# Kernel optimization log

Measured on AMD Instinct MI355X. Metric: run time of the kernel, lower is better.

Reference implementation:

```python
import jax, jax.numpy as jnp
import numpy as np

B, SQ, SKV = 4, 4096, 1024
QDIM, CDIM = 1024, 768
HEADS, DHEAD = 16, 64
INNER = HEADS * DHEAD


def setup_inputs() -> dict:
    key = jax.random.key(0)
    ks = jax.random.split(key, 7)
    s = 0.02
    return {
        "x": jax.random.normal(ks[0], (B, SQ, QDIM), dtype=jnp.float32),
        "context": jax.random.normal(ks[1], (B, SKV, CDIM), dtype=jnp.float32),
        "Wq": jax.random.normal(ks[2], (QDIM, INNER), dtype=jnp.float32) * s,
        "Wk": jax.random.normal(ks[3], (CDIM, INNER), dtype=jnp.float32) * s,
        "Wv": jax.random.normal(ks[4], (CDIM, INNER), dtype=jnp.float32) * s,
        "Wo": jax.random.normal(ks[5], (INNER, QDIM), dtype=jnp.float32) * s,
        "bo": jnp.zeros((QDIM,), dtype=jnp.float32),
    }


def reference(x, context, Wq, Wk, Wv, Wo, bo):
    # QKV projections (no bias, matching bias=False Linear layers)
    q = x @ Wq          # [B, SQ, INNER]
    k = context @ Wk    # [B, SKV, INNER]
    v = context @ Wv    # [B, SKV, INNER]

    # split heads: b s (h d) -> b h s d
    def split_heads(t, s):
        return t.reshape(B, s, HEADS, DHEAD).transpose(0, 2, 1, 3)

    qh = split_heads(q, SQ)
    kh = split_heads(k, SKV)
    vh = split_heads(v, SKV)

    scale = DHEAD ** -0.5  # attention_basic default scale
    sim = jnp.einsum('bhqd,bhkd->bhqk', qh, kh) * scale  # [B,H,SQ,SKV]
    attn = jax.nn.softmax(sim, axis=-1)
    out = jnp.einsum('bhqk,bhkd->bhqd', attn, vh)        # [B,H,SQ,DHEAD]
    out = out.transpose(0, 2, 1, 3).reshape(B, SQ, INNER)

    # output projection (Linear with bias); dropout p=0 -> identity
    return out @ Wo + bo
```

## Files before the change

### kernel.cpp

```cpp
#include <hip/hip_runtime.h>


typedef unsigned short u16;
typedef unsigned int u32;
typedef __bf16 bf16x8 __attribute__((ext_vector_type(8)));
typedef float float4v __attribute__((ext_vector_type(4)));
typedef _Float16 half4 __attribute__((ext_vector_type(4)));
typedef _Float16 half2v __attribute__((ext_vector_type(2)));
typedef __attribute__((address_space(1))) void as1_void;
typedef __attribute__((address_space(3))) void as3_void;

__device__ __forceinline__ u16 f2bf(float f) {
  unsigned u = __float_as_uint(f);
  u += 0x7FFF + ((u >> 16) & 1);
  return (u16)(u >> 16);
}

__device__ __forceinline__ void async16(const u16* g, u16* l) {
  __builtin_amdgcn_global_load_lds((as1_void*)(void*)g, (as3_void*)l, 16, 0, 0);
}

#define WAITCNT_VM8 0xF78
#define WAITCNT_VM4 0xF74
#define WAITCNT_VM0 0xF70

__global__ void cvt_kernel(const float* __restrict__ x, u16* __restrict__ xbf,
                           const float* __restrict__ ctx, u16* __restrict__ ctxbf) {
  int i = blockIdx.x * 256 + threadIdx.x;
  const float* in; u16* out; int j;
  if (i < 4194304) { in = x; out = xbf; j = i; }
  else if (i < 4980736) { in = ctx; out = ctxbf; j = i - 4194304; }
  else return;
  float4 v = ((const float4*)in)[j];
  ushort4 o;
  o.x = f2bf(v.x); o.y = f2bf(v.y); o.z = f2bf(v.z); o.w = f2bf(v.w);
  ((ushort4*)out)[j] = o;
}

__global__ void twt_kernel(const float* __restrict__ Wq, const float* __restrict__ Wk,
                           const float* __restrict__ Wv, const float* __restrict__ Wo,
                           u16* __restrict__ WqT, u16* __restrict__ WkT,
                           u16* __restrict__ WvT, u16* __restrict__ WoT) {
  __shared__ u16 t[32][33];
  int z = blockIdx.z;
  const float* W = z == 0 ? Wq : z == 1 ? Wk : z == 2 ? Wv : Wo;
  u16* Wt = z == 0 ? WqT : z == 1 ? WkT : z == 2 ? WvT : WoT;
  int Kd = (z == 1 || z == 2) ? 768 : 1024;
  int k0 = blockIdx.y * 32;
  if (k0 >= Kd) return;
  int tx = threadIdx.x, ty = threadIdx.y;
  int n0 = blockIdx.x * 32;
#pragma unroll
  for (int i = 0; i < 4; i++)
    t[ty + i * 8][tx] = f2bf(W[(size_t)(k0 + ty + i * 8) * 1024 + n0 + tx]);
  __syncthreads();
#pragma unroll
  for (int i = 0; i < 4; i++)
    Wt[(size_t)(n0 + ty + i * 8) * Kd + k0 + tx] = t[tx][ty + i * 8];
}


__device__ __forceinline__ void ld_a4(const u16* Lp, int rbase, int quad,
                                      int l15, bf16x8 a[4][2]) {
  int lb = l15 & 7;
  const char* base = (const char*)Lp;
#pragma unroll
  for (int mi = 0; mi < 4; mi++)
#pragma unroll
    for (int ks = 0; ks < 2; ks++)
      a[mi][ks] = *(const bf16x8*)(base + (rbase + mi * 16 + l15) * 128 +
                                   (((ks * 4 + quad) ^ lb) << 4));
}

__device__ __forceinline__ void ld_b2(const u16* Lp, int rbase, int quad,
                                      int l15, bf16x8 b[2][2]) {
  int lb = l15 & 7;
  const char* base = (const char*)Lp;
#pragma unroll
  for (int ni = 0; ni < 2; ni++)
#pragma unroll
    for (int ks = 0; ks < 2; ks++)
      b[ni][ks] = *(const bf16x8*)(base + (rbase + ni * 16 + l15) * 128 +
                                   (((ks * 4 + quad) ^ lb) << 4));
}

__device__ __forceinline__ void mm16(bf16x8 a[4][2], bf16x8 b[2][2],
                                     float4v acc[8][4], int mh, int nh) {
  __builtin_amdgcn_s_setprio(1);
#pragma unroll
  for (int mi = 0; mi < 4; mi++)
#pragma unroll
    for (int ni = 0; ni < 2; ni++)
#pragma unroll
      for (int ks = 0; ks < 2; ks++)
        acc[mh * 4 + mi][nh * 2 + ni] = __builtin_amdgcn_mfma_f32_16x16x32_bf16(
            a[mi][ks], b[ni][ks], acc[mh * 4 + mi][nh * 2 + ni], 0, 0, 0);
  __builtin_amdgcn_s_setprio(0);
}

__device__ __forceinline__ void gemm256_core(const u16* __restrict__ A,
                                             const u16* __restrict__ Bt, int K,
                                             int m0, int n0, float4v acc[8][4]) {
  __shared__ __align__(16) u16 L[2][2][256][64];
  int tid = threadIdx.x;
  int w = tid >> 6, lane = tid & 63;
  int l15 = lane & 15, quad = lane >> 4;
  int wm = (w >> 2) * 128, wn = (w & 3) * 64;

  int lr = lane >> 3, sl = lane & 7;
  const u16* pA = A + (size_t)(m0 + (w << 5) + lr) * K + ((sl ^ lr) << 3);
  const u16* pB = Bt + (size_t)(n0 + (w << 5) + lr) * K + ((sl ^ lr) << 3);
  size_t r8 = (size_t)K << 3;
  int dofs = (w << 11) + lane * 8;

#define STG_A(buf, t)                                                          \
  do {                                                                         \
    const u16* s = pA + (size_t)(t) * 64;                                      \
    u16* d = &L[buf][0][0][0] + dofs;                                          \
    async16(s, d);                                                             \
    async16(s + r8, d + 512);                                                  \
    async16(s + 2 * r8, d + 1024);                                             \
    async16(s + 3 * r8, d + 1536);                                             \
  } while (0)
#define STG_B(buf, t)                                                          \
  do {                                                                         \
    const u16* s = pB + (size_t)(t) * 64;                                      \
    u16* d = &L[buf][1][0][0] + dofs;                                          \
    async16(s, d);                                                             \
    async16(s + r8, d + 512);                                                  \
    async16(s + 2 * r8, d + 1024);                                             \
    async16(s + 3 * r8, d + 1536);                                             \
  } while (0)

  STG_A(0, 0); STG_B(0, 0);
  STG_A(1, 1); STG_B(1, 1);
  __builtin_amdgcn_s_waitcnt(WAITCNT_VM8);
  __builtin_amdgcn_s_barrier();

  bf16x8 a[4][2], b0[2][2], b1[2][2];
  int I = K >> 7;
  for (int i = 0; i < I; ++i) {
    int st = (i + 1 < I);
    ld_a4(&L[0][0][0][0], wm, quad, l15, a);
    ld_b2(&L[0][1][0][0], wn, quad, l15, b0);
    if (i > 0) STG_B(1, 2 * i + 1);
    __builtin_amdgcn_s_barrier();
    mm16(a, b0, acc, 0, 0);
    __builtin_amdgcn_s_barrier();
    ld_b2(&L[0][1][0][0], wn + 32, quad, l15, b1);
    __builtin_amdgcn_s_barrier();
    mm16(a, b1, acc, 0, 1);
    __builtin_amdgcn_s_barrier();
    ld_a4(&L[0][0][0][0], wm + 64, quad, l15, a);
    __builtin_amdgcn_s_barrier();
    mm16(a, b1, acc, 1, 1);
    __builtin_amdgcn_s_barrier();
    if (st) STG_A(0, 2 * i + 2);
    __builtin_amdgcn_s_barrier();
    mm16(a, b0, acc, 1, 0);
    if (st) __builtin_amdgcn_s_waitcnt(WAITCNT_VM4);
    else    __builtin_amdgcn_s_waitcnt(WAITCNT_VM0);
    __builtin_amdgcn_s_barrier();
    ld_a4(&L[1][0][0][0], wm, quad, l15, a);
    ld_b2(&L[1][1][0][0], wn, quad, l15, b0);
    if (st) STG_B(0, 2 * i + 2);
    __builtin_amdgcn_s_barrier();
    mm16(a, b0, acc, 0, 0);
    __builtin_amdgcn_s_barrier();
    ld_b2(&L[1][1][0][0], wn + 32, quad, l15, b1);
    __builtin_amdgcn_s_barrier();
    mm16(a, b1, acc, 0, 1);
    __builtin_amdgcn_s_barrier();
    ld_a4(&L[1][0][0][0], wm + 64, quad, l15, a);
    __builtin_amdgcn_s_barrier();
    mm16(a, b1, acc, 1, 1);
    __builtin_amdgcn_s_barrier();
    if (st) STG_A(1, 2 * i + 3);
    __builtin_amdgcn_s_barrier();
    mm16(a, b0, acc, 1, 0);
    if (st) __builtin_amdgcn_s_waitcnt(WAITCNT_VM4);
    __builtin_amdgcn_s_barrier();
  }
#undef STG_A
#undef STG_B
}

__global__ __launch_bounds__(512, 2) void qkv_gemm8(
    const u16* __restrict__ xbf, const u16* __restrict__ ctxbf,
    const u16* __restrict__ WqT, const u16* __restrict__ WkT, const u16* __restrict__ WvT,
    u16* __restrict__ Qb, u16* __restrict__ Kbuf, u16* __restrict__ Vtb, float qscale) {
  int bx0 = blockIdx.x;
  int bx = (bx0 & 7) * 48 + (bx0 >> 3);
  const u16* A; const u16* Bt; u16* C; int K, mode, m0, n0; float scale;
  if (bx < 256)      { int t = bx;       A = xbf;   Bt = WqT; C = Qb;   K = 1024; mode = 0; scale = qscale; m0 = (t >> 2) * 256; n0 = (t & 3) * 256; }
  else if (bx < 320) { int t = bx - 256; A = ctxbf; Bt = WkT; C = Kbuf; K = 768;  mode = 0; scale = 1.0f;   m0 = (t >> 2) * 256; n0 = (t & 3) * 256; }
  else               { int t = bx - 320; A = ctxbf; Bt = WvT; C = Vtb;  K = 768;  mode = 2; scale = 1.0f;   m0 = (t >> 2) * 256; n0 = (t & 3) * 256; }

  float4v acc[8][4] = {};
  gemm256_core(A, Bt, K, m0, n0, acc);

  int tid = threadIdx.x;
  int w = tid >> 6, lane = tid & 63;
  int l15 = lane & 15, quad = lane >> 4;
  int wm = (w >> 2) * 128, wn = (w & 3) * 64;

  if (mode == 0) {
#pragma unroll
    for (int mi = 0; mi < 8; mi++) {
      int rowb = m0 + wm + mi * 16 + quad * 4;
#pragma unroll
      for (int ni = 0; ni < 4; ni++) {
        int col = n0 + wn + ni * 16 + l15;
#pragma unroll
        for (int r = 0; r < 4; r++)
          C[(size_t)(rowb + r) * 1024 + col] = f2bf(acc[mi][ni][r] * scale);
      }
    }
  } else {
#pragma unroll
    for (int mi = 0; mi < 8; mi++) {
      int rowb = m0 + wm + mi * 16 + quad * 4;
#pragma unroll
      for (int ni = 0; ni < 4; ni++) {
        int col = n0 + wn + ni * 16 + l15;
        int hh = col >> 6, dd = col & 63;
#pragma unroll
        for (int r = 0; r < 4; r++) {
          int rr = rowb + r;
          int b = rr >> 10, skv = rr & 1023;
          _Float16 hv = (_Float16)acc[mi][ni][r];
          C[((((size_t)b * 16 + hh) * 64 + dd) << 10) + skv] = __builtin_bit_cast(u16, hv);
        }
      }
    }
  }
}

__global__ __launch_bounds__(512, 2) void gemm_bt8(
    const u16* __restrict__ A, const u16* __restrict__ Bt,
    float* __restrict__ C, const float* __restrict__ bias) {
  int bx0 = blockIdx.x;
  int bx = (bx0 & 7) * 32 + (bx0 >> 3);
  int m0 = (bx >> 2) * 256, n0 = (bx & 3) * 256;

  float4v acc[8][4] = {};
  gemm256_core(A, Bt, 1024, m0, n0, acc);

  int tid = threadIdx.x;
  int w = tid >> 6, lane = tid & 63;
  int l15 = lane & 15, quad = lane >> 4;
  int wm = (w >> 2) * 128, wn = (w & 3) * 64;

#pragma unroll
  for (int mi = 0; mi < 8; mi++) {
    int rowb = m0 + wm + mi * 16 + quad * 4;
#pragma unroll
    for (int ni = 0; ni < 4; ni++) {
      int col = n0 + wn + ni * 16 + l15;
      float bv = bias[col];
#pragma unroll
      for (int r = 0; r < 4; r++)
        C[(size_t)(rowb + r) * 1024 + col] = acc[mi][ni][r] + bv;
    }
  }
}

__global__ __launch_bounds__(512, 4) void attn_kernel(
    const u16* __restrict__ Q, const u16* __restrict__ Kb,
    const u16* __restrict__ Vt, u16* __restrict__ Oout) {
  __shared__ __align__(16) u16 lK[2][8192];
  __shared__ __align__(16) u16 lV[2][8192];
  int tid = threadIdx.x, w = tid >> 6, lane = tid & 63;
  int l15 = lane & 15, quad = lane >> 4;
  int bh = blockIdx.y, b = bh >> 4, h = bh & 15;
  int q0 = blockIdx.x * 256 + w * 32;

  const u16* Qbase = Q + ((size_t)(b * 4096 + q0)) * 1024 + h * 64;
  const u16* Kbase = Kb + ((size_t)b << 20) + h * 64;
  const u16* Vbase = Vt + ((size_t)bh << 16);

  bf16x8 qf[2][2];
#pragma unroll
  for (int qt = 0; qt < 2; qt++)
#pragma unroll
    for (int c = 0; c < 2; c++)
      qf[qt][c] = *(const bf16x8*)(Qbase + (size_t)(qt * 16 + l15) * 1024 + c * 32 + quad * 8);

  int kr0 = tid >> 3, kx0 = ((tid & 7) ^ (kr0 & 7)) * 8;
  const u16* ks0 = Kbase + (size_t)kr0 * 1024 + kx0;
  const u16* ks1 = ks0 + (size_t)64 * 1024;
  int vd0 = tid >> 4, vc0 = ((tid & 15) ^ (vd0 & 15)) * 8;
  const u16* vs0 = Vbase + (size_t)vd0 * 1024 + vc0;
  const u16* vs1 = vs0 + (size_t)32 * 1024;
  int kdo0 = w * 512, kdo1 = 4096 + w * 512;

  async16(ks0, &lK[0][kdo0]); async16(ks1, &lK[0][kdo1]);
  async16(vs0, &lV[0][kdo0]); async16(vs1, &lV[0][kdo1]);
  ks0 += 131072; ks1 += 131072;
  vs0 += 128; vs1 += 128;

  float4v o[2][4] = {};
  float4v osum[2] = {};
  const half4 ones = {(_Float16)1.0f, (_Float16)1.0f, (_Float16)1.0f, (_Float16)1.0f};

  int lb = l15 & 7;
  int xk0 = ((0 + quad) ^ lb) * 16 + l15 * 128;
  int xk1 = ((4 + quad) ^ lb) * 16 + l15 * 128;
  int qh = quad >> 1, qo = (quad & 1) * 8;
  int vrow = l15 * 256 + qo;

  for (int it = 0; it < 8; ++it) {
    const char* bK = (const char*)lK + (it & 1) * 16384;
    const char* bV = (const char*)lV + (it & 1) * 16384;
    __syncthreads();
    if (it < 7) {
      int nb = (it + 1) & 1;
      async16(ks0, &lK[nb][kdo0]); async16(ks1, &lK[nb][kdo1]);
      async16(vs0, &lV[nb][kdo0]); async16(vs1, &lV[nb][kdo1]);
      ks0 += 131072; ks1 += 131072;
      vs0 += 128; vs1 += 128;
    }
#pragma unroll
    for (int ss = 0; ss < 8; ss++) {
      int sub = (ss + w) & 7;
      int sb = sub * 2048;
      float4v sv[2] = {{0.f, 0.f, 0.f, 0.f}, {0.f, 0.f, 0.f, 0.f}};
      __builtin_amdgcn_s_setprio(1);
#pragma unroll
      for (int c = 0; c < 2; c++) {
        bf16x8 kf = *(const bf16x8*)(bK + sb + (c ? xk1 : xk0));
#pragma unroll
        for (int qt = 0; qt < 2; qt++)
          sv[qt] = __builtin_amdgcn_mfma_f32_16x16x32_bf16(kf, qf[qt][c], sv[qt], 0, 0, 0);
      }
      __builtin_amdgcn_s_setprio(0);
      half4 pf[2];
#pragma unroll
      for (int qt = 0; qt < 2; qt++) {
        float e0 = exp2f(sv[qt][0]), e1 = exp2f(sv[qt][1]);
        float e2 = exp2f(sv[qt][2]), e3 = exp2f(sv[qt][3]);
        half2v p01 = __builtin_bit_cast(half2v, __builtin_amdgcn_cvt_pkrtz(e0, e1));
        half2v p23 = __builtin_bit_cast(half2v, __builtin_amdgcn_cvt_pkrtz(e2, e3));
        pf[qt] = __builtin_shufflevector(p01, p23, 0, 1, 2, 3);
        osum[qt] = __builtin_amdgcn_mfma_f32_16x16x16f16(ones, pf[qt], osum[qt], 0, 0, 0);
      }
      int vbs = vrow + (((sub * 2 + qh) ^ l15) * 16);
      __builtin_amdgcn_s_setprio(1);
#pragma unroll
      for (int dt = 0; dt < 4; dt++) {
        half4 vf = *(const half4*)(bV + dt * 4096 + vbs);
#pragma unroll
        for (int qt = 0; qt < 2; qt++)
          o[qt][dt] = __builtin_amdgcn_mfma_f32_16x16x16f16(vf, pf[qt], o[qt][dt], 0, 0, 0);
      }
      __builtin_amdgcn_s_setprio(0);
    }
  }

#pragma unroll
  for (int qt = 0; qt < 2; qt++) {
    float inv = 1.0f / osum[qt][0];
    u16* Ob = Oout + ((size_t)(b * 4096 + q0 + qt * 16 + l15)) * 1024 + h * 64 + quad * 4;
#pragma unroll
    for (int dt = 0; dt < 4; dt++) {
      ushort4 pk;
      pk.x = f2bf(o[qt][dt][0] * inv);
      pk.y = f2bf(o[qt][dt][1] * inv);
      pk.z = f2bf(o[qt][dt][2] * inv);
      pk.w = f2bf(o[qt][dt][3] * inv);
      *(ushort4*)(Ob + dt * 16) = pk;
    }
  }
}

extern "C" void kernel_launch(void* const* d_in, const int* in_sizes, int n_in,
                              void* d_out, int out_size, void* d_ws, size_t ws_size,
                              hipStream_t stream) {
  const float* x   = (const float*)d_in[0];
  const float* ctx = (const float*)d_in[1];
  const float* Wq  = (const float*)d_in[2];
  const float* Wk  = (const float*)d_in[3];
  const float* Wv  = (const float*)d_in[4];
  const float* Wo  = (const float*)d_in[5];
  const float* bo  = (const float*)d_in[6];
  float* out = (float*)d_out;

  u16* ws    = (u16*)d_ws;
  u16* xbf   = ws;
  u16* ctxbf = xbf + 16777216;
  u16* WqT   = ctxbf + 3145728;
  u16* WkT   = WqT + 1048576;
  u16* WvT   = WkT + 786432;
  u16* WoT   = WvT + 786432;
  u16* Qb    = WoT + 1048576;
  u16* Kbuf  = Qb + 16777216;
  u16* Vtb   = Kbuf + 4194304;
  if (ws_size < (size_t)48758784 * 2) return;

  cvt_kernel<<<19456, 256, 0, stream>>>(x, xbf, ctx, ctxbf);
  twt_kernel<<<dim3(32, 32, 4), dim3(32, 8), 0, stream>>>(Wq, Wk, Wv, Wo, WqT, WkT, WvT, WoT);
  qkv_gemm8<<<dim3(384), dim3(512), 0, stream>>>(xbf, ctxbf, WqT, WkT, WvT,
                                                 Qb, Kbuf, Vtb, 0.18033688011112042f);
  attn_kernel<<<dim3(16, 64), dim3(512), 0, stream>>>(Qb, Kbuf, Vtb, xbf);
  gemm_bt8<<<dim3(256), dim3(512), 0, stream>>>(xbf, WoT, out, bo);
}
```

Baseline: 342.0 us.

## Merge prep kernels and software-pipeline QK^T MFMA ahead of softmax in attention

Combines the fp32-to-bf16 conversion and weight transpose kernels into a single launch, saving one kernel launch and its tail. In the attention inner loop, the QK^T scores for the next 16-key subtile are computed before the exp/PV work on the current subtile. This lets MFMA latency overlap with the exp2 transcendentals. The cost is extra live registers (svn/svc), which may raise register pressure.

```diff
diff --git a/kernel.cpp b/kernel.cpp
--- a/kernel.cpp
+++ b/kernel.cpp
@@ -24,32 +24,37 @@
 #define WAITCNT_VM4 0xF74
 #define WAITCNT_VM0 0xF70
 
-__global__ void cvt_kernel(const float* __restrict__ x, u16* __restrict__ xbf,
-                           const float* __restrict__ ctx, u16* __restrict__ ctxbf) {
-  int i = blockIdx.x * 256 + threadIdx.x;
-  const float* in; u16* out; int j;
-  if (i < 4194304) { in = x; out = xbf; j = i; }
-  else if (i < 4980736) { in = ctx; out = ctxbf; j = i - 4194304; }
-  else return;
-  float4 v = ((const float4*)in)[j];
-  ushort4 o;
-  o.x = f2bf(v.x); o.y = f2bf(v.y); o.z = f2bf(v.z); o.w = f2bf(v.w);
-  ((ushort4*)out)[j] = o;
-}
-
-__global__ void twt_kernel(const float* __restrict__ Wq, const float* __restrict__ Wk,
-                           const float* __restrict__ Wv, const float* __restrict__ Wo,
-                           u16* __restrict__ WqT, u16* __restrict__ WkT,
-                           u16* __restrict__ WvT, u16* __restrict__ WoT) {
+__global__ void prep_kernel(const float* __restrict__ x, u16* __restrict__ xbf,
+                            const float* __restrict__ ctx, u16* __restrict__ ctxbf,
+                            const float* __restrict__ Wq, const float* __restrict__ Wk,
+                            const float* __restrict__ Wv, const float* __restrict__ Wo,
+                            u16* __restrict__ WqT, u16* __restrict__ WkT,
+                            u16* __restrict__ WvT, u16* __restrict__ WoT) {
   __shared__ u16 t[32][33];
-  int z = blockIdx.z;
+  int blk = blockIdx.x;
+  if (blk < 19456) {
+    int i = blk * 256 + threadIdx.x;
+    const float* in; u16* out; int j;
+    if (i < 4194304) { in = x; out = xbf; j = i; }
+    else if (i < 4980736) { in = ctx; out = ctxbf; j = i - 4194304; }
+    else return;
+    float4 v = ((const float4*)in)[j];
+    ushort4 o;
+    o.x = f2bf(v.x); o.y = f2bf(v.y); o.z = f2bf(v.z); o.w = f2bf(v.w);
+    ((ushort4*)out)[j] = o;
+    return;
+  }
+  int rem = blk - 19456;
+  int z = rem >> 10, r1 = rem & 1023;
+  int by = r1 >> 5, bxx = r1 & 31;
   const float* W = z == 0 ? Wq : z == 1 ? Wk : z == 2 ? Wv : Wo;
   u16* Wt = z == 0 ? WqT : z == 1 ? WkT : z == 2 ? WvT : WoT;
   int Kd = (z == 1 || z == 2) ? 768 : 1024;
-  int k0 = blockIdx.y * 32;
+  int k0 = by * 32;
   if (k0 >= Kd) return;
-  int tx = threadIdx.x, ty = threadIdx.y;
-  int n0 = blockIdx.x * 32;
+  int tid = threadIdx.x;
+  int tx = tid & 31, ty = tid >> 5;
+  int n0 = bxx * 32;
 #pragma unroll
   for (int i = 0; i < 4; i++)
     t[ty + i * 8][tx] = f2bf(W[(size_t)(k0 + ty + i * 8) * 1024 + n0 + tx]);
@@ -320,25 +325,40 @@
       ks0 += 131072; ks1 += 131072;
       vs0 += 128; vs1 += 128;
     }
+    float4v svc[2] = {{0.f, 0.f, 0.f, 0.f}, {0.f, 0.f, 0.f, 0.f}};
+    {
+      int sb0 = (w & 7) * 2048;
+      __builtin_amdgcn_s_setprio(1);
+#pragma unroll
+      for (int c = 0; c < 2; c++) {
+        bf16x8 kf = *(const bf16x8*)(bK + sb0 + (c ? xk1 : xk0));
+#pragma unroll
+        for (int qt = 0; qt < 2; qt++)
+          svc[qt] = __builtin_amdgcn_mfma_f32_16x16x32_bf16(kf, qf[qt][c], svc[qt], 0, 0, 0);
+      }
+      __builtin_amdgcn_s_setprio(0);
+    }
 #pragma unroll
     for (int ss = 0; ss < 8; ss++) {
       int sub = (ss + w) & 7;
-      int sb = sub * 2048;
-      float4v sv[2] = {{0.f, 0.f, 0.f, 0.f}, {0.f, 0.f, 0.f, 0.f}};
-      __builtin_amdgcn_s_setprio(1);
-#pragma unroll
-      for (int c = 0; c < 2; c++) {
-        bf16x8 kf = *(const bf16x8*)(bK + sb + (c ? xk1 : xk0));
-#pragma unroll
-        for (int qt = 0; qt < 2; qt++)
-          sv[qt] = __builtin_amdgcn_mfma_f32_16x16x32_bf16(kf, qf[qt][c], sv[qt], 0, 0, 0);
-      }
-      __builtin_amdgcn_s_setprio(0);
+      float4v svn[2] = {{0.f, 0.f, 0.f, 0.f}, {0.f, 0.f, 0.f, 0.f}};
+      if (ss < 7) {
+        int sbn = ((ss + 1 + w) & 7) * 2048;
+        __builtin_amdgcn_s_setprio(1);
+#pragma unroll
+        for (int c = 0; c < 2; c++) {
+          bf16x8 kf = *(const bf16x8*)(bK + sbn + (c ? xk1 : xk0));
+#pragma unroll
+          for (int qt = 0; qt < 2; qt++)
+            svn[qt] = __builtin_amdgcn_mfma_f32_16x16x32_bf16(kf, qf[qt][c], svn[qt], 0, 0, 0);
+        }
+        __builtin_amdgcn_s_setprio(0);
+      }
       half4 pf[2];
 #pragma unroll
       for (int qt = 0; qt < 2; qt++) {
-        float e0 = exp2f(sv[qt][0]), e1 = exp2f(sv[qt][1]);
-        float e2 = exp2f(sv[qt][2]), e3 = exp2f(sv[qt][3]);
+        float e0 = exp2f(svc[qt][0]), e1 = exp2f(svc[qt][1]);
+        float e2 = exp2f(svc[qt][2]), e3 = exp2f(svc[qt][3]);
         half2v p01 = __builtin_bit_cast(half2v, __builtin_amdgcn_cvt_pkrtz(e0, e1));
         half2v p23 = __builtin_bit_cast(half2v, __builtin_amdgcn_cvt_pkrtz(e2, e3));
         pf[qt] = __builtin_shufflevector(p01, p23, 0, 1, 2, 3);
@@ -354,6 +374,8 @@
           o[qt][dt] = __builtin_amdgcn_mfma_f32_16x16x16f16(vf, pf[qt], o[qt][dt], 0, 0, 0);
       }
       __builtin_amdgcn_s_setprio(0);
+      svc[0] = svn[0];
+      svc[1] = svn[1];
     }
   }
 
@@ -397,8 +419,8 @@
   u16* Vtb   = Kbuf + 4194304;
   if (ws_size < (size_t)48758784 * 2) return;
 
-  cvt_kernel<<<19456, 256, 0, stream>>>(x, xbf, ctx, ctxbf);
-  twt_kernel<<<dim3(32, 32, 4), dim3(32, 8), 0, stream>>>(Wq, Wk, Wv, Wo, WqT, WkT, WvT, WoT);
+  prep_kernel<<<23552, 256, 0, stream>>>(x, xbf, ctx, ctxbf,
+                                         Wq, Wk, Wv, Wo, WqT, WkT, WvT, WoT);
   qkv_gemm8<<<dim3(384), dim3(512), 0, stream>>>(xbf, ctxbf, WqT, WkT, WvT,
                                                  Qb, Kbuf, Vtb, 0.18033688011112042f);
   attn_kernel<<<dim3(16, 64), dim3(512), 0, stream>>>(Qb, Kbuf, Vtb, xbf);
```

Result: no change. 348.0 us (+1.8%).
